# Performance work log

Hardware: AMD Instinct MI355X
Metric: run time of the kernel (lower is better)

## Reference

```python
import jax, jax.numpy as jnp
import numpy as np

NUM_NODES = 100000
INPUT_DIM = 256
NUM_BAGS = 2048
BAG_SIZE = 64
N_EDGES = 3200000  # num_nodes * avg_degree(32)


def setup_inputs() -> dict:
    key = jax.random.key(0)
    ks = jax.random.split(key, 7)
    x = jax.random.normal(ks[0], (NUM_NODES, INPUT_DIM), dtype=jnp.float32)
    bags = jax.random.randint(ks[1], (NUM_BAGS, BAG_SIZE), 0, NUM_NODES)
    alpha_values = jax.random.uniform(ks[2], (NUM_BAGS, BAG_SIZE, 1), dtype=jnp.float32)
    # edge_dict in COO form: edge_src[e] has neighbor edge_nbr[e]
    edge_src = jax.random.randint(ks[3], (N_EDGES,), 0, NUM_NODES)
    edge_nbr = jax.random.randint(ks[4], (N_EDGES,), 0, NUM_NODES)
    node_weights = jax.random.uniform(ks[5], (NUM_NODES,), dtype=jnp.float32)  # torch.rand init
    theta_w = jax.random.normal(ks[6], (INPUT_DIM,), dtype=jnp.float32) / np.sqrt(INPUT_DIM)
    return dict(x=x, bags=bags, alpha_values=alpha_values, edge_src=edge_src,
                edge_nbr=edge_nbr, node_weights=node_weights, theta_w=theta_w)


def reference(x, bags, alpha_values, edge_src, edge_nbr, node_weights, theta_w):
    # Per-source neighbor weight sum: sum_value(source) = sum(node_weights[edge_dict[source]])
    nbr_sum = jax.ops.segment_sum(node_weights[edge_nbr], edge_src, num_segments=NUM_NODES)
    deg = jax.ops.segment_sum(jnp.ones_like(edge_src, dtype=x.dtype), edge_src,
                              num_segments=NUM_NODES)
    # sources not in edge_dict get sum_value = 1.0
    nbr_sum = jnp.where(deg > 0, nbr_sum, jnp.asarray(1.0, x.dtype))
    # h_values = theta(x[bag]); theta is Linear(input_dim, 1, bias=False)
    h = jnp.einsum('nbd,d->nb', x[bags], theta_w)          # [num_bags, bag_size]
    feat = h * alpha_values[..., 0]                         # [num_bags, bag_size]
    ns = nbr_sum[bags]                                      # [num_bags, bag_size]
    return jnp.sum(ns * feat, axis=1)                       # [num_bags]
```

## Files before the change

### kernel.cpp

```cpp
#include <hip/hip_runtime.h>

#define NUM_NODES 100000
#define INPUT_DIM 256
#define NUM_BAGS  2048
#define BAG_SIZE  64
#define N_EDGES   3200000
#define NQUAD     (N_EDGES / 4)

#define NPP3      33334
#define NSL3      85
#define QPS3      9412
#define NPP8      12500
#define NSL8      32
#define QPS8      (NQUAD / NSL8)

typedef unsigned int u32;
typedef float f4 __attribute__((ext_vector_type(4)));

__global__ void __launch_bounds__(256)
pack_edges(const int* __restrict__ edge_src, const int* __restrict__ edge_nbr,
           const float* __restrict__ nw, u32* __restrict__ packed) {
    const int q = blockIdx.x * 256 + threadIdx.x;
    const int4 s4 = ((const int4*)edge_src)[q];
    const int4 n4 = ((const int4*)edge_nbr)[q];
#define PACK(S, N)  (((u32)(S) << 15) |                                     \
                     (((__float_as_uint(nw[(N)]) + 0x8000u) >> 16) & 0x7FFFu))
    uint4 o;
    o.x = PACK(s4.x, n4.x);
    o.y = PACK(s4.y, n4.y);
    o.z = PACK(s4.z, n4.z);
    o.w = PACK(s4.w, n4.w);
#undef PACK
    ((uint4*)packed)[q] = o;
}

__global__ void __launch_bounds__(1024)
hist3(const u32* __restrict__ packed, float* __restrict__ rep) {
    extern __shared__ float hist[];
    const int p    = blockIdx.x / NSL3;
    const int b    = blockIdx.x % NSL3;
    const int base = p * NPP3;
    const int tid  = threadIdx.x;

    for (int j = tid; j < NPP3; j += 1024) hist[j] = 0.f;
    __syncthreads();

    const int lo = b * QPS3;
    const int hi = (lo + QPS3 < NQUAD) ? lo + QPS3 : NQUAD;
#define EDGE(W)                                                          \
        {                                                                \
            const u32 rel = ((W) >> 15) - (u32)base;                     \
            if (rel < (u32)NPP3)                                         \
                atomicAdd(&hist[rel],                                    \
                          __uint_as_float(((W) & 0x7FFFu) << 16));       \
        }
    for (int q = lo + tid; q < hi; q += 1024) {
        const uint4 a = ((const uint4*)packed)[q];
        EDGE(a.x) EDGE(a.y) EDGE(a.z) EDGE(a.w)
    }
#undef EDGE
    __syncthreads();

    const int nflush = (NUM_NODES - base < NPP3) ? NUM_NODES - base : NPP3;
    float* dst = rep + (size_t)b * NUM_NODES + base;
    for (int j = tid; j < nflush; j += 1024)
        __builtin_nontemporal_store(hist[j], &dst[j]);
}

__global__ void __launch_bounds__(1024)
hist_p(const u32* __restrict__ packed, float* __restrict__ rep) {
    __shared__ float hist[NPP8];
    const int i    = blockIdx.x;
    const int r    = i & 7;
    const int p    = (i >> 3) & 7;
    const int b    = r | ((i >> 6) << 3);
    const int base = p * NPP8;

    for (int j = threadIdx.x; j < NPP8 / 4; j += 1024)
        ((f4*)hist)[j] = (f4){0.f, 0.f, 0.f, 0.f};
    __syncthreads();

    const int lo = b * QPS8;
#define EDGE(W)                                                          \
        {                                                                \
            const u32 rel = ((W) >> 15) - (u32)base;                     \
            if (rel < (u32)NPP8)                                         \
                atomicAdd(&hist[rel],                                    \
                          __uint_as_float(((W) & 0x7FFFu) << 16));       \
        }
    for (int q = lo + (int)threadIdx.x; q < lo + QPS8; q += 1024) {
        const uint4 a = ((const uint4*)packed)[q];
        EDGE(a.x) EDGE(a.y) EDGE(a.z) EDGE(a.w)
    }
#undef EDGE
    __syncthreads();

    float* dst = rep + (size_t)b * NUM_NODES + base;
    for (int j = threadIdx.x; j < NPP8 / 4; j += 1024) {
        const f4 v = ((const f4*)hist)[j];
        __builtin_nontemporal_store(v, &((f4*)dst)[j]);
    }
}

#define RED_BLK 98
template <int NSL>
__global__ void __launch_bounds__(256)
gemv_reduce(const float* __restrict__ rep, float* __restrict__ nbr_sum,
            const float* __restrict__ x, const float* __restrict__ theta,
            float* __restrict__ h) {
    if (blockIdx.x < RED_BLK) {
        const int i = blockIdx.x * 256 + threadIdx.x;
        if (i >= NUM_NODES / 4) return;
        float4 a = make_float4(0.f, 0.f, 0.f, 0.f);
        #pragma unroll 5
        for (int r = 0; r < NSL; ++r) {
            const float4 v = ((const float4*)(rep + (size_t)r * NUM_NODES))[i];
            a.x += v.x; a.y += v.y; a.z += v.z; a.w += v.w;
        }
        float4 o;
        o.x = a.x > 0.f ? a.x : 1.0f;
        o.y = a.y > 0.f ? a.y : 1.0f;
        o.z = a.z > 0.f ? a.z : 1.0f;
        o.w = a.w > 0.f ? a.w : 1.0f;
        ((float4*)nbr_sum)[i] = o;
    } else {
        const int gb   = blockIdx.x - RED_BLK;
        const int lane = threadIdx.x & 63;
        const int wave = threadIdx.x >> 6;
        const float4 tw = *reinterpret_cast<const float4*>(&theta[lane * 4]);
        for (int row = gb * 4 + wave; row < NUM_NODES; row += 2048 * 4) {
            const float4 xv =
                *reinterpret_cast<const float4*>(&x[(size_t)row * INPUT_DIM + lane * 4]);
            float d = xv.x * tw.x + xv.y * tw.y + xv.z * tw.z + xv.w * tw.w;
            #pragma unroll
            for (int off = 32; off >= 1; off >>= 1)
                d += __shfl_xor(d, off);
            if (lane == 0) h[row] = d;
        }
    }
}

__global__ void __launch_bounds__(256)
bag_final(const int* __restrict__ bags, const float* __restrict__ alpha,
          const float* __restrict__ h, const float* __restrict__ ns,
          float* __restrict__ out) {
    const int bag  = blockIdx.x * 4 + (threadIdx.x >> 6);
    const int lane = threadIdx.x & 63;
    const int idx  = bags[bag * BAG_SIZE + lane];
    float v = h[idx] * ns[idx] * alpha[bag * BAG_SIZE + lane];
    #pragma unroll
    for (int off = 32; off >= 1; off >>= 1)
        v += __shfl_xor(v, off);
    if (lane == 0) out[bag] = v;
}

__global__ void __launch_bounds__(256)
edge_atomic(const int* __restrict__ edge_src, const int* __restrict__ edge_nbr,
            const float* __restrict__ nw, float* __restrict__ nbr_sum) {
    const int t = blockIdx.x * blockDim.x + threadIdx.x;
    const int4 s4 = ((const int4*)edge_src)[t];
    const int4 n4 = ((const int4*)edge_nbr)[t];
    atomicAdd(&nbr_sum[s4.x], nw[n4.x]);
    atomicAdd(&nbr_sum[s4.y], nw[n4.y]);
    atomicAdd(&nbr_sum[s4.z], nw[n4.z]);
    atomicAdd(&nbr_sum[s4.w], nw[n4.w]);
}

__global__ void __launch_bounds__(256)
fixup_nosum(float* __restrict__ nbr_sum) {
    const int i = blockIdx.x * 256 + threadIdx.x;
    if (i < NUM_NODES && nbr_sum[i] == 0.f) nbr_sum[i] = 1.0f;
}

__global__ void __launch_bounds__(256)
gemv_h(const float* __restrict__ x, const float* __restrict__ theta,
       float* __restrict__ h) {
    const int lane = threadIdx.x & 63;
    const int wave = threadIdx.x >> 6;
    const float4 tw = *reinterpret_cast<const float4*>(&theta[lane * 4]);
    const int stride = gridDim.x * 4;
    for (int row = blockIdx.x * 4 + wave; row < NUM_NODES; row += stride) {
        const float4 xv =
            *reinterpret_cast<const float4*>(&x[(size_t)row * INPUT_DIM + lane * 4]);
        float d = xv.x * tw.x + xv.y * tw.y + xv.z * tw.z + xv.w * tw.w;
        #pragma unroll
        for (int off = 32; off >= 1; off >>= 1)
            d += __shfl_xor(d, off);
        if (lane == 0) h[row] = d;
    }
}

extern "C" void kernel_launch(void* const* d_in, const int* in_sizes, int n_in,
                              void* d_out, int out_size, void* d_ws, size_t ws_size,
                              hipStream_t stream) {
    const float* x            = (const float*)d_in[0];
    const int*   bags         = (const int*)d_in[1];
    const float* alpha        = (const float*)d_in[2];
    const int*   edge_src     = (const int*)d_in[3];
    const int*   edge_nbr     = (const int*)d_in[4];
    const float* node_weights = (const float*)d_in[5];
    const float* theta        = (const float*)d_in[6];
    float*       out          = (float*)d_out;

    const size_t need3 =
        ((size_t)N_EDGES + (size_t)NSL3 * NUM_NODES + 2 * (size_t)NUM_NODES) * 4;
    const size_t need8 =
        ((size_t)N_EDGES + (size_t)NSL8 * NUM_NODES + 2 * (size_t)NUM_NODES) * 4;

    const hipError_t attr_ok = hipFuncSetAttribute(
        (const void*)hist3, hipFuncAttributeMaxDynamicSharedMemorySize,
        NPP3 * (int)sizeof(float));

    if (attr_ok == hipSuccess && ws_size >= need3) {
        u32*   packed  = (u32*)d_ws;
        float* rep     = (float*)d_ws + N_EDGES;
        float* nbr_sum = rep + (size_t)NSL3 * NUM_NODES;
        float* h       = nbr_sum + NUM_NODES;

        pack_edges<<<NQUAD / 256, 256, 0, stream>>>(edge_src, edge_nbr,
                                                    node_weights, packed);
        hist3<<<3 * NSL3, 1024, NPP3 * sizeof(float), stream>>>(packed, rep);
        gemv_reduce<NSL3><<<RED_BLK + 2048, 256, 0, stream>>>(rep, nbr_sum,
                                                              x, theta, h);
        bag_final<<<NUM_BAGS / 4, 256, 0, stream>>>(bags, alpha, h, nbr_sum, out);
    } else if (ws_size >= need8) {
        u32*   packed  = (u32*)d_ws;
        float* rep     = (float*)d_ws + N_EDGES;
        float* nbr_sum = rep + (size_t)NSL8 * NUM_NODES;
        float* h       = nbr_sum + NUM_NODES;

        pack_edges<<<NQUAD / 256, 256, 0, stream>>>(edge_src, edge_nbr,
                                                    node_weights, packed);
        hist_p<<<8 * NSL8, 1024, 0, stream>>>(packed, rep);
        gemv_reduce<NSL8><<<RED_BLK + 2048, 256, 0, stream>>>(rep, nbr_sum,
                                                              x, theta, h);
        bag_final<<<NUM_BAGS / 4, 256, 0, stream>>>(bags, alpha, h, nbr_sum, out);
    } else {
        float* nbr_sum = (float*)d_ws;
        float* h       = nbr_sum + NUM_NODES;
        hipMemsetAsync(nbr_sum, 0, (size_t)NUM_NODES * 4, stream);
        edge_atomic<<<(N_EDGES / 4) / 256, 256, 0, stream>>>(
            edge_src, edge_nbr, node_weights, nbr_sum);
        fixup_nosum<<<(NUM_NODES + 255) / 256, 256, 0, stream>>>(nbr_sum);
        gemv_h<<<2048, 256, 0, stream>>>(x, theta, h);
        bag_final<<<NUM_BAGS / 4, 256, 0, stream>>>(bags, alpha, h, nbr_sum, out);
    }
}
```

Before: 73.96 us.

## Store partial histograms as bf16, use 4x64 split, skip GEMV rows not in bags

The main path now splits the per-node histogram into 4 node partitions and 64 edge slices. Partial sums are written as packed bf16 instead of fp32, which halves the intermediate write and read traffic. A new mark_used pass flags the nodes that appear in any bag, and the GEMV skips x rows that are not flagged, avoiding reads of x rows that never reach the output. This adds a memset and an extra kernel launch, and rounding each partial to bf16 adds error to the neighbour sums.

```diff
diff --git a/kernel.cpp b/kernel.cpp
--- a/kernel.cpp
+++ b/kernel.cpp
@@ -7,15 +7,17 @@
 #define N_EDGES   3200000
 #define NQUAD     (N_EDGES / 4)
 
-#define NPP3      33334
-#define NSL3      85
-#define QPS3      9412
+#define NPP4      25000
+#define NSL4      64
+#define QPS4      (NQUAD / NSL4)
 #define NPP8      12500
 #define NSL8      32
 #define QPS8      (NQUAD / NSL8)
 
 typedef unsigned int u32;
+typedef unsigned short u16;
 typedef float f4 __attribute__((ext_vector_type(4)));
+typedef u32   u4 __attribute__((ext_vector_type(4)));
 
 __global__ void __launch_bounds__(256)
 pack_edges(const int* __restrict__ edge_src, const int* __restrict__ edge_nbr,
@@ -35,36 +37,42 @@
 }
 
 __global__ void __launch_bounds__(1024)
-hist3(const u32* __restrict__ packed, float* __restrict__ rep) {
+hist4(const u32* __restrict__ packed, u16* __restrict__ rep16) {
     extern __shared__ float hist[];
-    const int p    = blockIdx.x / NSL3;
-    const int b    = blockIdx.x % NSL3;
-    const int base = p * NPP3;
-    const int tid  = threadIdx.x;
-
-    for (int j = tid; j < NPP3; j += 1024) hist[j] = 0.f;
+    const int p    = blockIdx.x & 3;
+    const int b    = blockIdx.x >> 2;
+    const int base = p * NPP4;
+
+    for (int j = threadIdx.x; j < NPP4 / 4; j += 1024)
+        ((f4*)hist)[j] = (f4){0.f, 0.f, 0.f, 0.f};
     __syncthreads();
 
-    const int lo = b * QPS3;
-    const int hi = (lo + QPS3 < NQUAD) ? lo + QPS3 : NQUAD;
+    const int lo = b * QPS4;
 #define EDGE(W)                                                          \
         {                                                                \
             const u32 rel = ((W) >> 15) - (u32)base;                     \
-            if (rel < (u32)NPP3)                                         \
+            if (rel < (u32)NPP4)                                         \
                 atomicAdd(&hist[rel],                                    \
                           __uint_as_float(((W) & 0x7FFFu) << 16));       \
         }
-    for (int q = lo + tid; q < hi; q += 1024) {
+    for (int q = lo + (int)threadIdx.x; q < lo + QPS4; q += 1024) {
         const uint4 a = ((const uint4*)packed)[q];
         EDGE(a.x) EDGE(a.y) EDGE(a.z) EDGE(a.w)
     }
 #undef EDGE
     __syncthreads();
 
-    const int nflush = (NUM_NODES - base < NPP3) ? NUM_NODES - base : NPP3;
-    float* dst = rep + (size_t)b * NUM_NODES + base;
-    for (int j = tid; j < nflush; j += 1024)
-        __builtin_nontemporal_store(hist[j], &dst[j]);
+    u16* dst = rep16 + (size_t)b * NUM_NODES + base;
+    for (int j = threadIdx.x; j < NPP4 / 8; j += 1024) {
+        u4 v;
+        #pragma unroll
+        for (int k = 0; k < 4; ++k) {
+            const u32 lo_b = (__float_as_uint(hist[j * 8 + 2 * k])     + 0x8000u) >> 16;
+            const u32 hi_b = (__float_as_uint(hist[j * 8 + 2 * k + 1]) + 0x8000u) >> 16;
+            v[k] = lo_b | (hi_b << 16);
+        }
+        __builtin_nontemporal_store(v, &((u4*)dst)[j]);
+    }
 }
 
 __global__ void __launch_bounds__(1024)
@@ -102,8 +110,60 @@
     }
 }
 
+__global__ void __launch_bounds__(256)
+mark_used(const int* __restrict__ bags, unsigned char* __restrict__ used) {
+    const int i = blockIdx.x * 256 + threadIdx.x;
+    used[bags[i]] = 1;
+}
+
+#define RED4 49
+__global__ void __launch_bounds__(256)
+gemv_reduce4(const u16* __restrict__ rep16, float* __restrict__ nbr_sum,
+             const float* __restrict__ x, const float* __restrict__ theta,
+             float* __restrict__ h, const unsigned char* __restrict__ used) {
+    if (blockIdx.x < RED4) {
+        const int g = blockIdx.x * 256 + threadIdx.x;
+        if (g >= NUM_NODES / 8) return;
+        float acc[8] = {0.f, 0.f, 0.f, 0.f, 0.f, 0.f, 0.f, 0.f};
+        #pragma unroll 4
+        for (int r = 0; r < NSL4; ++r) {
+            const u4 v = ((const u4*)(rep16 + (size_t)r * NUM_NODES))[g];
+            #pragma unroll
+            for (int k = 0; k < 4; ++k) {
+                acc[2 * k]     += __uint_as_float(v[k] << 16);
+                acc[2 * k + 1] += __uint_as_float(v[k] & 0xFFFF0000u);
+            }
+        }
+        float4 o0, o1;
+        o0.x = acc[0] > 0.f ? acc[0] : 1.0f;
+        o0.y = acc[1] > 0.f ? acc[1] : 1.0f;
+        o0.z = acc[2] > 0.f ? acc[2] : 1.0f;
+        o0.w = acc[3] > 0.f ? acc[3] : 1.0f;
+        o1.x = acc[4] > 0.f ? acc[4] : 1.0f;
+        o1.y = acc[5] > 0.f ? acc[5] : 1.0f;
+        o1.z = acc[6] > 0.f ? acc[6] : 1.0f;
+        o1.w = acc[7] > 0.f ? acc[7] : 1.0f;
+        ((float4*)nbr_sum)[2 * g]     = o0;
+        ((float4*)nbr_sum)[2 * g + 1] = o1;
+    } else {
+        const int gb   = blockIdx.x - RED4;
+        const int lane = threadIdx.x & 63;
+        const int wave = threadIdx.x >> 6;
+        const float4 tw = *reinterpret_cast<const float4*>(&theta[lane * 4]);
+        for (int row = gb * 4 + wave; row < NUM_NODES; row += 2048 * 4) {
+            if (!used[row]) continue;
+            const float4 xv =
+                *reinterpret_cast<const float4*>(&x[(size_t)row * INPUT_DIM + lane * 4]);
+            float d = xv.x * tw.x + xv.y * tw.y + xv.z * tw.z + xv.w * tw.w;
+            #pragma unroll
+            for (int off = 32; off >= 1; off >>= 1)
+                d += __shfl_xor(d, off);
+            if (lane == 0) h[row] = d;
+        }
+    }
+}
+
 #define RED_BLK 98
-template <int NSL>
 __global__ void __launch_bounds__(256)
 gemv_reduce(const float* __restrict__ rep, float* __restrict__ nbr_sum,
             const float* __restrict__ x, const float* __restrict__ theta,
@@ -112,8 +172,8 @@
         const int i = blockIdx.x * 256 + threadIdx.x;
         if (i >= NUM_NODES / 4) return;
         float4 a = make_float4(0.f, 0.f, 0.f, 0.f);
-        #pragma unroll 5
-        for (int r = 0; r < NSL; ++r) {
+        #pragma unroll 8
+        for (int r = 0; r < NSL8; ++r) {
             const float4 v = ((const float4*)(rep + (size_t)r * NUM_NODES))[i];
             a.x += v.x; a.y += v.y; a.z += v.z; a.w += v.w;
         }
@@ -202,26 +262,29 @@
     const float* theta        = (const float*)d_in[6];
     float*       out          = (float*)d_out;
 
-    const size_t need3 =
-        ((size_t)N_EDGES + (size_t)NSL3 * NUM_NODES + 2 * (size_t)NUM_NODES) * 4;
+    const size_t need4 = (size_t)N_EDGES * 4 + (size_t)NSL4 * NUM_NODES * 2
+                       + 2 * (size_t)NUM_NODES * 4 + NUM_NODES;
     const size_t need8 =
         ((size_t)N_EDGES + (size_t)NSL8 * NUM_NODES + 2 * (size_t)NUM_NODES) * 4;
 
     const hipError_t attr_ok = hipFuncSetAttribute(
-        (const void*)hist3, hipFuncAttributeMaxDynamicSharedMemorySize,
-        NPP3 * (int)sizeof(float));
-
-    if (attr_ok == hipSuccess && ws_size >= need3) {
+        (const void*)hist4, hipFuncAttributeMaxDynamicSharedMemorySize,
+        NPP4 * (int)sizeof(float));
+
+    if (attr_ok == hipSuccess && ws_size >= need4) {
         u32*   packed  = (u32*)d_ws;
-        float* rep     = (float*)d_ws + N_EDGES;
-        float* nbr_sum = rep + (size_t)NSL3 * NUM_NODES;
+        u16*   rep16   = (u16*)(packed + N_EDGES);
+        float* nbr_sum = (float*)(rep16 + (size_t)NSL4 * NUM_NODES);
         float* h       = nbr_sum + NUM_NODES;
-
+        unsigned char* used = (unsigned char*)(h + NUM_NODES);
+
+        hipMemsetAsync(used, 0, NUM_NODES, stream);
+        mark_used<<<(NUM_BAGS * BAG_SIZE) / 256, 256, 0, stream>>>(bags, used);
         pack_edges<<<NQUAD / 256, 256, 0, stream>>>(edge_src, edge_nbr,
                                                     node_weights, packed);
-        hist3<<<3 * NSL3, 1024, NPP3 * sizeof(float), stream>>>(packed, rep);
-        gemv_reduce<NSL3><<<RED_BLK + 2048, 256, 0, stream>>>(rep, nbr_sum,
-                                                              x, theta, h);
+        hist4<<<4 * NSL4, 1024, NPP4 * sizeof(float), stream>>>(packed, rep16);
+        gemv_reduce4<<<RED4 + 2048, 256, 0, stream>>>(rep16, nbr_sum, x, theta,
+                                                      h, used);
         bag_final<<<NUM_BAGS / 4, 256, 0, stream>>>(bags, alpha, h, nbr_sum, out);
     } else if (ws_size >= need8) {
         u32*   packed  = (u32*)d_ws;
@@ -232,8 +295,7 @@
         pack_edges<<<NQUAD / 256, 256, 0, stream>>>(edge_src, edge_nbr,
                                                     node_weights, packed);
         hist_p<<<8 * NSL8, 1024, 0, stream>>>(packed, rep);
-        gemv_reduce<NSL8><<<RED_BLK + 2048, 256, 0, stream>>>(rep, nbr_sum,
-                                                              x, theta, h);
+        gemv_reduce<<<RED_BLK + 2048, 256, 0, stream>>>(rep, nbr_sum, x, theta, h);
         bag_final<<<NUM_BAGS / 4, 256, 0, stream>>>(bags, alpha, h, nbr_sum, out);
     } else {
         float* nbr_sum = (float*)d_ws;
```

Result: slower. 75.54 us (+2.1%).
